# Kernel optimization log

Measured on AMD Instinct MI355X. Metric: run time of the kernel, lower is better.

Reference implementation:

```python
import jax, jax.numpy as jnp
import numpy as np

NEG_SLOPE = 0.01  # F.leaky_relu default


def gcn_conv(x, W, b, src, dst):
    """PyG GCNConv: add self-loops, symmetric deg^-1/2 normalization, linear, scatter-add."""
    n = x.shape[0]
    loop = jnp.arange(n)
    s = jnp.concatenate([src, loop])  # source j
    d = jnp.concatenate([dst, loop])  # target i
    deg = jax.ops.segment_sum(jnp.ones_like(d, dtype=x.dtype), d, num_segments=n)
    dis = jnp.where(deg > 0, jax.lax.rsqrt(jnp.maximum(deg, 1e-12)), 0.0)
    norm = dis[s] * dis[d]                       # [E+N]
    h = x @ W                                    # [N, out]
    msg = h[s] * norm[:, None]                   # gather + scale
    out = jax.ops.segment_sum(msg, d, num_segments=n)  # scatter-add to targets
    return out + b


def setup_inputs() -> dict:
    key = jax.random.key(0)
    ks = jax.random.split(key, 8)
    N, E, G = 100000, 800000, 100
    IN, H, OUT = 128, 256, 16
    x = jax.random.normal(ks[0], (N, IN), dtype=jnp.float32)
    edge_index = jax.random.randint(ks[1], (2, E), 0, N, dtype=jnp.int64)
    batch = jnp.repeat(jnp.arange(G, dtype=jnp.int64), N // G)  # sorted graph ids
    def glorot(k, fi, fo):
        lim = np.sqrt(6.0 / (fi + fo))
        return jax.random.uniform(k, (fi, fo), jnp.float32, -lim, lim)
    return {
        "x": x, "edge_index": edge_index, "batch": batch,
        "W1": glorot(ks[2], IN, H), "b1": jnp.zeros((H,), jnp.float32),
        "W2": glorot(ks[3], H, H),  "b2": jnp.zeros((H,), jnp.float32),
        "W3": glorot(ks[4], H, OUT), "b3": jnp.zeros((OUT,), jnp.float32),
    }


def reference(x, edge_index, batch, W1, b1, W2, b2, W3, b3):
    src, dst = edge_index[0], edge_index[1]
    h = gcn_conv(x, W1, b1, src, dst)
    h = jax.nn.leaky_relu(h, NEG_SLOPE)  # dropout p=0.0 -> identity
    h = gcn_conv(h, W2, b2, src, dst)
    h = jax.nn.leaky_relu(h, NEG_SLOPE)
    h = gcn_conv(h, W3, b3, src, dst)
    # get_zero_nodes: first node of each graph in the sorted batch vector
    mask = jnp.concatenate([jnp.array([True]), batch[1:] != batch[:-1]])
    return h[mask, :]  # [n_graphs, out_channels]
```

## Files before the change

kernel.cpp:

```cpp
#include <hip/hip_runtime.h>

#define NEG_SLOPE 0.01f

using short8 = __attribute__((ext_vector_type(8))) short;
using f32x4  = __attribute__((ext_vector_type(4))) float;

__device__ inline float b2f(ushort u) {
    union { unsigned u; float f; } x; x.u = ((unsigned)u) << 16; return x.f;
}
__device__ inline ushort f2b(float f) {
    union { float f; unsigned u; } x; x.f = f;
    unsigned r = x.u + 0x7FFFu + ((x.u >> 16) & 1u);
    return (ushort)(r >> 16);
}
__device__ inline void gload16(const void* g, void* l) {
    __builtin_amdgcn_global_load_lds((__attribute__((address_space(1))) void*)g,
                                     (__attribute__((address_space(3))) void*)l, 16, 0, 0);
}


__global__ void init_kernel(const int* __restrict__ batch, int* __restrict__ cnt,
                            int* __restrict__ flag1, int* __restrict__ flag2,
                            int* __restrict__ rootflag, int* __restrict__ picked, int N) {
    int i = blockIdx.x * blockDim.x + threadIdx.x;
    if (i >= N) return;
    cnt[i] = 0;
    int root = (i == 0) || (batch[i] != batch[i - 1]);
    flag1[i] = root;
    flag2[i] = 0;
    rootflag[i] = root;
    if (root) picked[batch[i]] = i;
}


__global__ void count_f1(const int* __restrict__ src, const int* __restrict__ dst,
                         const int* __restrict__ rootflag, int* __restrict__ cnt,
                         int* __restrict__ flag1, int E) {
    int i = blockIdx.x * blockDim.x + threadIdx.x;
    int e0 = i * 4;
    if (e0 + 3 < E) {
        int4 dq = *(const int4*)(dst + e0);
        int r0 = rootflag[dq.x], r1 = rootflag[dq.y], r2 = rootflag[dq.z], r3 = rootflag[dq.w];
        atomicAdd(&cnt[dq.x], 1);
        atomicAdd(&cnt[dq.y], 1);
        atomicAdd(&cnt[dq.z], 1);
        atomicAdd(&cnt[dq.w], 1);
        if (r0 | r1 | r2 | r3) {
            int4 sq = *(const int4*)(src + e0);
            if (r0) flag1[sq.x] = 1;
            if (r1) flag1[sq.y] = 1;
            if (r2) flag1[sq.z] = 1;
            if (r3) flag1[sq.w] = 1;
        }
    } else if (e0 < E) {
        for (int e = e0; e < E; e++) {
            int d = dst[e];
            atomicAdd(&cnt[d], 1);
            if (rootflag[d]) flag1[src[e]] = 1;
        }
    }
}


__global__ void frontier2v(const int* __restrict__ src, const int* __restrict__ dst,
                           const int* __restrict__ flag1, int* __restrict__ flag2,
                           int E, int N) {
    int i = blockIdx.x * blockDim.x + threadIdx.x;
    int e0 = i * 4;
    if (e0 + 3 < E) {
        int4 dq = *(const int4*)(dst + e0);
        int f0 = flag1[dq.x], f1 = flag1[dq.y], f2 = flag1[dq.z], f3 = flag1[dq.w];
        if (f0 | f1 | f2 | f3) {
            int4 sq = *(const int4*)(src + e0);
            if (f0) flag2[sq.x] = 1;
            if (f1) flag2[sq.y] = 1;
            if (f2) flag2[sq.z] = 1;
            if (f3) flag2[sq.w] = 1;
        }
    } else if (e0 < E) {
        for (int e = e0; e < E; e++) if (flag1[dst[e]]) flag2[src[e]] = 1;
    }
    if (i < N && flag1[i]) flag2[i] = 1;
}


__global__ __launch_bounds__(256) void tscan1w(const int* __restrict__ cnt,
                                               const int* __restrict__ f1,
                                               const int* __restrict__ f2,
                                               int4* __restrict__ bsums,
                                               float* __restrict__ dis, int N, int nb,
                                               const float* __restrict__ W1, ushort* __restrict__ W1t,
                                               const float* __restrict__ W2, ushort* __restrict__ W2t) {
    __shared__ int l0[256], l1[256], l2[256];
    int b = blockIdx.x, t = threadIdx.x;
    if (b < nb) {
        int base = b * 1024 + t * 4;
        int c[4] = {0,0,0,0}, a1[4] = {0,0,0,0}, a2[4] = {0,0,0,0};
        if (base + 3 < N) {
            int4 q = *(const int4*)(cnt + base); c[0]=q.x; c[1]=q.y; c[2]=q.z; c[3]=q.w;
            int4 u = *(const int4*)(f1 + base);  a1[0]=u.x; a1[1]=u.y; a1[2]=u.z; a1[3]=u.w;
            int4 v = *(const int4*)(f2 + base);  a2[0]=v.x; a2[1]=v.y; a2[2]=v.z; a2[3]=v.w;
        } else {
            for (int i = 0; i < 4; i++) if (base + i < N) {
                c[i] = cnt[base + i]; a1[i] = f1[base + i]; a2[i] = f2[base + i];
            }
        }
#pragma unroll
        for (int i = 0; i < 4; i++)
            if (base + i < N) dis[base + i] = rsqrtf((float)c[i] + 1.0f);
        int s0 = 0, s1 = 0, s2 = 0;
#pragma unroll
        for (int i = 0; i < 4; i++) { s0 += a2[i] ? c[i] : 0; s1 += a1[i]; s2 += a2[i]; }
        l0[t] = s0; l1[t] = s1; l2[t] = s2;
        __syncthreads();
        for (int off = 128; off > 0; off >>= 1) {
            if (t < off) { l0[t] += l0[t + off]; l1[t] += l1[t + off]; l2[t] += l2[t + off]; }
            __syncthreads();
        }
        if (t == 0) bsums[b] = make_int4(l0[0], l1[0], l2[0], 0);
    }
    for (int idx = b * 256 + t; idx < 98304; idx += gridDim.x * 256) {
        if (idx < 32768) {
            int n = idx >> 7, k = idx & 127;
            W1t[idx] = f2b(W1[k * 256 + n]);
        } else {
            int j = idx - 32768;
            int n = j >> 8, k = j & 255;
            W2t[j] = f2b(W2[k * 256 + n]);
        }
    }
}

__global__ __launch_bounds__(1024) void tscan2(int4* __restrict__ bsums, int* __restrict__ counts,
                                               int* __restrict__ rowptr, int N, int nb) {
    __shared__ int l0[1024], l1[1024], l2[1024];
    int t = threadIdx.x;
    int v0 = 0, v1 = 0, v2 = 0;
    if (t < nb) { int4 v = bsums[t]; v0 = v.x; v1 = v.y; v2 = v.z; }
    l0[t] = v0; l1[t] = v1; l2[t] = v2;
    __syncthreads();
    for (int off = 1; off < 1024; off <<= 1) {
        int u0 = (t >= off) ? l0[t - off] : 0;
        int u1 = (t >= off) ? l1[t - off] : 0;
        int u2 = (t >= off) ? l2[t - off] : 0;
        __syncthreads();
        l0[t] += u0; l1[t] += u1; l2[t] += u2;
        __syncthreads();
    }
    if (t < nb) bsums[t] = make_int4(l0[t] - v0, l1[t] - v1, l2[t] - v2, 0);
    if (t == 1023) {
        counts[0] = l1[1023];
        counts[1] = l2[1023];
        rowptr[N] = l0[1023];
    }
}

__global__ __launch_bounds__(256) void tscan3(const int* __restrict__ cnt,
                                              const int* __restrict__ f1,
                                              const int* __restrict__ f2,
                                              const int4* __restrict__ bsums,
                                              int* __restrict__ rowptr, int* __restrict__ cur,
                                              int* __restrict__ pos1, int* __restrict__ pos2,
                                              int* __restrict__ list1, int* __restrict__ list2,
                                              int N) {
    __shared__ int l0[256], l1[256], l2[256];
    int b = blockIdx.x, t = threadIdx.x;
    int base = b * 1024 + t * 4;
    int c[4] = {0,0,0,0}, a1[4] = {0,0,0,0}, a2[4] = {0,0,0,0};
    if (base + 3 < N) {
        int4 q = *(const int4*)(cnt + base); c[0]=q.x; c[1]=q.y; c[2]=q.z; c[3]=q.w;
        int4 u = *(const int4*)(f1 + base);  a1[0]=u.x; a1[1]=u.y; a1[2]=u.z; a1[3]=u.w;
        int4 v = *(const int4*)(f2 + base);  a2[0]=v.x; a2[1]=v.y; a2[2]=v.z; a2[3]=v.w;
    } else {
        for (int i = 0; i < 4; i++) if (base + i < N) {
            c[i] = cnt[base + i]; a1[i] = f1[base + i]; a2[i] = f2[base + i];
        }
    }
    int m[4];
#pragma unroll
    for (int i = 0; i < 4; i++) m[i] = a2[i] ? c[i] : 0;
    int s0 = m[0] + m[1] + m[2] + m[3];
    int s1 = a1[0] + a1[1] + a1[2] + a1[3];
    int s2 = a2[0] + a2[1] + a2[2] + a2[3];
    l0[t] = s0; l1[t] = s1; l2[t] = s2;
    __syncthreads();
    for (int off = 1; off < 256; off <<= 1) {
        int u0 = (t >= off) ? l0[t - off] : 0;
        int u1 = (t >= off) ? l1[t - off] : 0;
        int u2 = (t >= off) ? l2[t - off] : 0;
        __syncthreads();
        l0[t] += u0; l1[t] += u1; l2[t] += u2;
        __syncthreads();
    }
    int4 bs = bsums[b];
    int run0 = bs.x + l0[t] - s0;
    int run1 = bs.y + l1[t] - s1;
    int run2 = bs.z + l2[t] - s2;
#pragma unroll
    for (int i = 0; i < 4; i++) {
        if (base + i < N) {
            rowptr[base + i] = run0;
            cur[base + i] = run0;
            if (a1[i]) { pos1[base + i] = run1; list1[run1] = base + i; }
            if (a2[i]) { pos2[base + i] = run2; list2[run2] = base + i; }
        }
        run0 += m[i]; run1 += a1[i]; run2 += a2[i];
    }
}


__global__ void fill_fv(const int* __restrict__ src, const int* __restrict__ dst,
                        const int* __restrict__ flag2, int* __restrict__ cur,
                        int* __restrict__ col, int E) {
    int i = blockIdx.x * blockDim.x + threadIdx.x;
    int e0 = i * 4;
    if (e0 + 3 < E) {
        int4 dq = *(const int4*)(dst + e0);
        int f0 = flag2[dq.x], f1 = flag2[dq.y], f2 = flag2[dq.z], f3 = flag2[dq.w];
        if (f0 | f1 | f2 | f3) {
            int4 sq = *(const int4*)(src + e0);
            if (f0) col[atomicAdd(&cur[dq.x], 1)] = sq.x;
            if (f1) col[atomicAdd(&cur[dq.y], 1)] = sq.y;
            if (f2) col[atomicAdd(&cur[dq.z], 1)] = sq.z;
            if (f3) col[atomicAdd(&cur[dq.w], 1)] = sq.w;
        }
    } else if (e0 < E) {
        for (int e = e0; e < E; e++) {
            int d = dst[e];
            if (flag2[d]) col[atomicAdd(&cur[d], 1)] = src[e];
        }
    }
}


__global__ __launch_bounds__(256) void aggx_c(const float* __restrict__ x,
                                              const float* __restrict__ dis,
                                              const int* __restrict__ rowptr,
                                              const int* __restrict__ col,
                                              const int* __restrict__ list2,
                                              const int* __restrict__ counts,
                                              ushort* __restrict__ aggXc) {
    const int M2 = counts[1];
    int wave = blockIdx.x * 4 + (threadIdx.x >> 6);
    int lane = threadIdx.x & 63;
    int li = lane & 31, sub = lane >> 5;
    int stride = gridDim.x * 8;
    const float* xp = x + li * 4;
    for (int p = wave * 2 + sub; p < M2; p += stride) {
        int node = list2[p];
        float di = dis[node];
        float4 sv = *(const float4*)(xp + (size_t)node * 128);
        float a0 = di * sv.x, a1 = di * sv.y, a2 = di * sv.z, a3 = di * sv.w;
        int e = rowptr[node], e1 = rowptr[node + 1];
        for (; e + 2 <= e1; e += 2) {
            int s0 = col[e], s1 = col[e + 1];
            float w0 = dis[s0], w1 = dis[s1];
            float4 v0 = *(const float4*)(xp + (size_t)s0 * 128);
            float4 v1 = *(const float4*)(xp + (size_t)s1 * 128);
            a0 += w0 * v0.x + w1 * v1.x;
            a1 += w0 * v0.y + w1 * v1.y;
            a2 += w0 * v0.z + w1 * v1.z;
            a3 += w0 * v0.w + w1 * v1.w;
        }
        if (e < e1) {
            int s = col[e];
            float w = dis[s];
            float4 v = *(const float4*)(xp + (size_t)s * 128);
            a0 += w * v.x; a1 += w * v.y; a2 += w * v.z; a3 += w * v.w;
        }
        ushort4 o;
        o.x = f2b(di * a0); o.y = f2b(di * a1); o.z = f2b(di * a2); o.w = f2b(di * a3);
        *(ushort4*)(aggXc + (size_t)p * 128 + li * 4) = o;
    }
}


__global__ __launch_bounds__(256) void agg2_c(const ushort* __restrict__ h1c,
                                              const float* __restrict__ dis,
                                              const int* __restrict__ rowptr,
                                              const int* __restrict__ col,
                                              const int* __restrict__ list1,
                                              const int* __restrict__ pos2,
                                              const int* __restrict__ counts,
                                              ushort* __restrict__ agg1c) {
    const int M1 = counts[0];
    int wave = blockIdx.x * 4 + (threadIdx.x >> 6);
    int lane = threadIdx.x & 63;
    int li = lane & 31, sub = lane >> 5;
    int stride = gridDim.x * 8;
    const ushort* hp = h1c + (size_t)li * 8;
    for (int p = wave * 2 + sub; p < M1; p += stride) {
        int i = list1[p];
        float di = dis[i];
        float a[8];
        {
            short8 v = *(const short8*)(hp + (size_t)pos2[i] * 256);
#pragma unroll
            for (int j = 0; j < 8; j++) a[j] = b2f((ushort)v[j]);
        }
        int e1 = rowptr[i + 1];
        for (int e = rowptr[i]; e < e1; e++) {
            short8 v = *(const short8*)(hp + (size_t)pos2[col[e]] * 256);
#pragma unroll
            for (int j = 0; j < 8; j++) a[j] += b2f((ushort)v[j]);
        }
        short8 o;
#pragma unroll
        for (int j = 0; j < 8; j++) o[j] = (short)f2b(di * a[j]);
        *(short8*)(agg1c + (size_t)p * 256 + li * 8) = o;
    }
}


template <int K>
__global__ __launch_bounds__(512) void gemm_c(const ushort* __restrict__ A,
                                              const ushort* __restrict__ Bt,
                                              const float* __restrict__ bias,
                                              const float* __restrict__ dis,
                                              const int* __restrict__ list,
                                              const int* __restrict__ counts, int which,
                                              ushort* __restrict__ C) {
    __shared__ ushort As[128 * 64];
    __shared__ ushort Bs[256 * 64];
    const int M = counts[which];
    const int t = threadIdx.x;
    const int lane = t & 63;
    const int w = t >> 6;
    const int wm = w >> 2, wn = w & 3;

    for (int tile = blockIdx.x; tile * 128 < M; tile += gridDim.x) {
        const int row0 = tile * 128;
        f32x4 acc[4][4] = {};

        for (int kt = 0; kt < K / 64; kt++) {
#pragma unroll
            for (int it = 0; it < 2; it++) {
                int q = it * 512 + t;
                int r = q >> 3, c = q & 7;
                int cs = c ^ (r & 7);
                int ga = min(row0 + r, M - 1);
                gload16(A + (size_t)ga * K + kt * 64 + cs * 8, &As[q * 8]);
            }
#pragma unroll
            for (int it = 0; it < 4; it++) {
                int q = it * 512 + t;
                int r = q >> 3, c = q & 7;
                int cs = c ^ (r & 7);
                gload16(Bt + (size_t)r * K + kt * 64 + cs * 8, &Bs[q * 8]);
            }
            __syncthreads();
#pragma unroll
            for (int ks = 0; ks < 2; ks++) {
                short8 a[4], b[4];
                int cc = ks * 4 + (lane >> 4);
#pragma unroll
                for (int m = 0; m < 4; m++) {
                    int R = wm * 64 + m * 16 + (lane & 15);
                    a[m] = *(const short8*)&As[R * 64 + ((cc ^ (R & 7)) * 8)];
                }
#pragma unroll
                for (int n = 0; n < 4; n++) {
                    int R = wn * 64 + n * 16 + (lane & 15);
                    b[n] = *(const short8*)&Bs[R * 64 + ((cc ^ (R & 7)) * 8)];
                }
#pragma unroll
                for (int m = 0; m < 4; m++)
#pragma unroll
                    for (int n = 0; n < 4; n++)
                        acc[m][n] = __builtin_amdgcn_mfma_f32_16x16x32_bf16(a[m], b[n], acc[m][n], 0, 0, 0);
            }
            __syncthreads();
        }

#pragma unroll
        for (int m = 0; m < 4; m++) {
#pragma unroll
            for (int j = 0; j < 4; j++) {
                int grow = row0 + wm * 64 + m * 16 + (lane >> 4) * 4 + j;
                if (grow >= M) continue;
                float dr = dis[list[grow]];
#pragma unroll
                for (int n = 0; n < 4; n++) {
                    int gcol = wn * 64 + n * 16 + (lane & 15);
                    float v = acc[m][n][j] + bias[gcol];
                    v = v > 0.f ? v : NEG_SLOPE * v;
                    C[(size_t)grow * 256 + gcol] = f2b(v * dr);
                }
            }
        }
    }
}


__global__ __launch_bounds__(256) void final_c(const ushort* __restrict__ h2c,
                                               const float* __restrict__ dis,
                                               const int* __restrict__ rowptr,
                                               const int* __restrict__ col,
                                               const int* __restrict__ picked,
                                               const int* __restrict__ pos1,
                                               const float* __restrict__ W3,
                                               const float* __restrict__ b3,
                                               float* __restrict__ out, int G) {
    __shared__ float agg[256];
    __shared__ float red[256];
    int g = blockIdx.x;
    int t = threadIdx.x;
    if (g >= G) return;
    int i = picked[g];
    float di = dis[i];
    float a = b2f(h2c[(size_t)pos1[i] * 256 + t]);
    int e1 = rowptr[i + 1];
    for (int e = rowptr[i]; e < e1; e++) {
        a += b2f(h2c[(size_t)pos1[col[e]] * 256 + t]);
    }
    agg[t] = di * a;
    __syncthreads();
    int c = t & 15, seg = t >> 4;
    float p = 0.f;
#pragma unroll
    for (int kk = 0; kk < 16; kk++) {
        int k = seg * 16 + kk;
        p += agg[k] * W3[k * 16 + c];
    }
    red[t] = p;
    __syncthreads();
    if (t < 16) {
        float sres = 0.f;
#pragma unroll
        for (int ss = 0; ss < 16; ss++) sres += red[ss * 16 + t];
        out[g * 16 + t] = sres + b3[t];
    }
}


extern "C" void kernel_launch(void* const* d_in, const int* in_sizes, int n_in,
                              void* d_out, int out_size, void* d_ws, size_t ws_size,
                              hipStream_t stream) {
    const float* x   = (const float*)d_in[0];
    const int* ei    = (const int*)d_in[1];
    const int* batch = (const int*)d_in[2];
    const float* W1  = (const float*)d_in[3];
    const float* b1  = (const float*)d_in[4];
    const float* W2  = (const float*)d_in[5];
    const float* b2  = (const float*)d_in[6];
    const float* W3  = (const float*)d_in[7];
    const float* b3  = (const float*)d_in[8];

    const int IN = 128, H = 256, OUT = 16;
    int N = in_sizes[0] / IN;
    int E = in_sizes[1] / 2;
    int G = out_size / OUT;
    const int* srcp = ei;
    const int* dstp = ei + E;

    char* p = (char*)d_ws;
    auto carve = [&](size_t bytes) {
        char* q = p;
        p += (bytes + 255) & ~(size_t)255;
        return q;
    };
    int*    cnt      = (int*)carve((size_t)N * 4);
    int*    flag1    = (int*)carve((size_t)N * 4);
    int*    flag2    = (int*)carve((size_t)N * 4);
    int*    rootflag = (int*)carve((size_t)N * 4);
    float*  dis    = (float*)carve((size_t)N * 4);
    int*    rowptr = (int*)carve(((size_t)N + 1) * 4);
    int*    cur    = (int*)carve((size_t)N * 4);
    int4*   tbsums = (int4*)carve(1024 * 16);
    int*    counts = (int*)carve(256);
    int*    picked = (int*)carve((size_t)G * 4);
    int*    pos1   = (int*)carve((size_t)N * 4);
    int*    pos2   = (int*)carve((size_t)N * 4);
    int*    list1  = (int*)carve((size_t)N * 4);
    int*    list2  = (int*)carve((size_t)N * 4);
    int*    col    = (int*)carve((size_t)E * 4);
    ushort* W1t    = (ushort*)carve((size_t)256 * 128 * 2);
    ushort* W2t    = (ushort*)carve((size_t)256 * 256 * 2);
    ushort* RA     = (ushort*)carve((size_t)N * H * 2);
    ushort* RB     = (ushort*)carve((size_t)N * H * 2);

    ushort* aggXc = RA;
    ushort* agg1c = RA;
    ushort* h1c   = RB;
    ushort* h2c   = RB;

    int nb = (N + 1023) / 1024;
    int e4 = (E + 3) / 4;
    int epN = (e4 > N ? e4 : N);
    int scanw_grid = (nb > 384 ? nb : 384);

    init_kernel<<<(N + 255) / 256, 256, 0, stream>>>(batch, cnt, flag1, flag2, rootflag, picked, N);

    count_f1<<<(e4 + 255) / 256, 256, 0, stream>>>(srcp, dstp, rootflag, cnt, flag1, E);

    frontier2v<<<(epN + 255) / 256, 256, 0, stream>>>(srcp, dstp, flag1, flag2, E, N);

    tscan1w<<<scanw_grid, 256, 0, stream>>>(cnt, flag1, flag2, tbsums, dis, N, nb, W1, W1t, W2, W2t);
    tscan2<<<1, 1024, 0, stream>>>(tbsums, counts, rowptr, N, nb);
    tscan3<<<nb, 256, 0, stream>>>(cnt, flag1, flag2, tbsums, rowptr, cur, pos1, pos2, list1, list2, N);

    fill_fv<<<(e4 + 255) / 256, 256, 0, stream>>>(srcp, dstp, flag2, cur, col, E);

    aggx_c<<<1024, 256, 0, stream>>>(x, dis, rowptr, col, list2, counts, aggXc);
    gemm_c<128><<<256, 512, 0, stream>>>(aggXc, W1t, b1, dis, list2, counts, 1, h1c);

    agg2_c<<<128, 256, 0, stream>>>(h1c, dis, rowptr, col, list1, pos2, counts, agg1c);
    gemm_c<256><<<64, 512, 0, stream>>>(agg1c, W2t, b2, dis, list1, counts, 0, h2c);

    final_c<<<G, 256, 0, stream>>>(h2c, dis, rowptr, col, picked, pos1, W3, b3, (float*)d_out, G);
}
```

Baseline: 134.1 us.

## Fuse three-pass scan into single-pass decoupled lookback scan

```diff
diff --git a/kernel.cpp b/kernel.cpp
--- a/kernel.cpp
+++ b/kernel.cpp
@@ -21,8 +21,10 @@
 
 __global__ void init_kernel(const int* __restrict__ batch, int* __restrict__ cnt,
                             int* __restrict__ flag1, int* __restrict__ flag2,
-                            int* __restrict__ rootflag, int* __restrict__ picked, int N) {
+                            int* __restrict__ rootflag, int* __restrict__ picked,
+                            int4* __restrict__ aggslot, int N) {
     int i = blockIdx.x * blockDim.x + threadIdx.x;
+    if (i < 1024) aggslot[i] = make_int4(0, 0, 0, 0);
     if (i >= N) return;
     cnt[i] = 0;
     int root = (i == 0) || (batch[i] != batch[i - 1]);
@@ -84,41 +86,101 @@
 }
 
 
-__global__ __launch_bounds__(256) void tscan1w(const int* __restrict__ cnt,
-                                               const int* __restrict__ f1,
-                                               const int* __restrict__ f2,
-                                               int4* __restrict__ bsums,
-                                               float* __restrict__ dis, int N, int nb,
-                                               const float* __restrict__ W1, ushort* __restrict__ W1t,
-                                               const float* __restrict__ W2, ushort* __restrict__ W2t) {
+__global__ __launch_bounds__(256) void scan_one(
+    const int* __restrict__ cnt, const int* __restrict__ f1, const int* __restrict__ f2,
+    int4* __restrict__ aggslot, float* __restrict__ dis,
+    int* __restrict__ rowptr, int* __restrict__ cur,
+    int* __restrict__ pos1, int* __restrict__ pos2,
+    int* __restrict__ list1, int* __restrict__ list2,
+    int* __restrict__ counts, int N, int nb,
+    const float* __restrict__ W1, ushort* __restrict__ W1t,
+    const float* __restrict__ W2, ushort* __restrict__ W2t) {
     __shared__ int l0[256], l1[256], l2[256];
-    int b = blockIdx.x, t = threadIdx.x;
-    if (b < nb) {
-        int base = b * 1024 + t * 4;
-        int c[4] = {0,0,0,0}, a1[4] = {0,0,0,0}, a2[4] = {0,0,0,0};
-        if (base + 3 < N) {
-            int4 q = *(const int4*)(cnt + base); c[0]=q.x; c[1]=q.y; c[2]=q.z; c[3]=q.w;
-            int4 u = *(const int4*)(f1 + base);  a1[0]=u.x; a1[1]=u.y; a1[2]=u.z; a1[3]=u.w;
-            int4 v = *(const int4*)(f2 + base);  a2[0]=v.x; a2[1]=v.y; a2[2]=v.z; a2[3]=v.w;
-        } else {
-            for (int i = 0; i < 4; i++) if (base + i < N) {
-                c[i] = cnt[base + i]; a1[i] = f1[base + i]; a2[i] = f2[base + i];
+    __shared__ int baseS[3];
+    const int b = blockIdx.x, t = threadIdx.x;
+    const int base = b * 1024 + t * 4;
+
+    int c[4] = {0,0,0,0}, a1[4] = {0,0,0,0}, a2[4] = {0,0,0,0};
+    if (base + 3 < N) {
+        int4 q = *(const int4*)(cnt + base); c[0]=q.x; c[1]=q.y; c[2]=q.z; c[3]=q.w;
+        int4 u = *(const int4*)(f1 + base);  a1[0]=u.x; a1[1]=u.y; a1[2]=u.z; a1[3]=u.w;
+        int4 v = *(const int4*)(f2 + base);  a2[0]=v.x; a2[1]=v.y; a2[2]=v.z; a2[3]=v.w;
+    } else {
+        for (int i = 0; i < 4; i++) if (base + i < N) {
+            c[i] = cnt[base + i]; a1[i] = f1[base + i]; a2[i] = f2[base + i];
+        }
+    }
+#pragma unroll
+    for (int i = 0; i < 4; i++)
+        if (base + i < N) dis[base + i] = rsqrtf((float)c[i] + 1.0f);
+
+    int m[4];
+#pragma unroll
+    for (int i = 0; i < 4; i++) m[i] = a2[i] ? c[i] : 0;
+    int ts0 = m[0] + m[1] + m[2] + m[3];
+    int ts1 = a1[0] + a1[1] + a1[2] + a1[3];
+    int ts2 = a2[0] + a2[1] + a2[2] + a2[3];
+    l0[t] = ts0; l1[t] = ts1; l2[t] = ts2;
+    __syncthreads();
+    for (int off = 1; off < 256; off <<= 1) {
+        int u0 = (t >= off) ? l0[t - off] : 0;
+        int u1 = (t >= off) ? l1[t - off] : 0;
+        int u2 = (t >= off) ? l2[t - off] : 0;
+        __syncthreads();
+        l0[t] += u0; l1[t] += u1; l2[t] += u2;
+        __syncthreads();
+    }
+
+    if (t == 0) {
+        __hip_atomic_store(&aggslot[b].x, l0[255], __ATOMIC_RELAXED, __HIP_MEMORY_SCOPE_AGENT);
+        __hip_atomic_store(&aggslot[b].y, l1[255], __ATOMIC_RELAXED, __HIP_MEMORY_SCOPE_AGENT);
+        __hip_atomic_store(&aggslot[b].z, l2[255], __ATOMIC_RELAXED, __HIP_MEMORY_SCOPE_AGENT);
+        __hip_atomic_store(&aggslot[b].w, 1, __ATOMIC_RELEASE, __HIP_MEMORY_SCOPE_AGENT);
+    }
+
+    if (t < 64) {
+        int g0 = 0, g1 = 0, g2 = 0;
+        for (int w0 = 0; w0 < b; w0 += 64) {
+            int idx = w0 + t;
+            if (idx < b) {
+                while (__hip_atomic_load(&aggslot[idx].w, __ATOMIC_ACQUIRE,
+                                         __HIP_MEMORY_SCOPE_AGENT) == 0) {
+                    __builtin_amdgcn_s_sleep(1);
+                }
+                g0 += __hip_atomic_load(&aggslot[idx].x, __ATOMIC_RELAXED, __HIP_MEMORY_SCOPE_AGENT);
+                g1 += __hip_atomic_load(&aggslot[idx].y, __ATOMIC_RELAXED, __HIP_MEMORY_SCOPE_AGENT);
+                g2 += __hip_atomic_load(&aggslot[idx].z, __ATOMIC_RELAXED, __HIP_MEMORY_SCOPE_AGENT);
             }
         }
 #pragma unroll
-        for (int i = 0; i < 4; i++)
-            if (base + i < N) dis[base + i] = rsqrtf((float)c[i] + 1.0f);
-        int s0 = 0, s1 = 0, s2 = 0;
-#pragma unroll
-        for (int i = 0; i < 4; i++) { s0 += a2[i] ? c[i] : 0; s1 += a1[i]; s2 += a2[i]; }
-        l0[t] = s0; l1[t] = s1; l2[t] = s2;
-        __syncthreads();
-        for (int off = 128; off > 0; off >>= 1) {
-            if (t < off) { l0[t] += l0[t + off]; l1[t] += l1[t + off]; l2[t] += l2[t + off]; }
-            __syncthreads();
-        }
-        if (t == 0) bsums[b] = make_int4(l0[0], l1[0], l2[0], 0);
-    }
+        for (int s = 1; s < 64; s <<= 1) {
+            g0 += __shfl_xor(g0, s, 64);
+            g1 += __shfl_xor(g1, s, 64);
+            g2 += __shfl_xor(g2, s, 64);
+        }
+        if (t == 0) { baseS[0] = g0; baseS[1] = g1; baseS[2] = g2; }
+    }
+    __syncthreads();
+
+    int run0 = baseS[0] + l0[t] - ts0;
+    int run1 = baseS[1] + l1[t] - ts1;
+    int run2 = baseS[2] + l2[t] - ts2;
+#pragma unroll
+    for (int i = 0; i < 4; i++) {
+        if (base + i < N) {
+            rowptr[base + i] = run0;
+            cur[base + i] = run0;
+            if (a1[i]) { pos1[base + i] = run1; list1[run1] = base + i; }
+            if (a2[i]) { pos2[base + i] = run2; list2[run2] = base + i; }
+        }
+        run0 += m[i]; run1 += a1[i]; run2 += a2[i];
+    }
+    if (b == nb - 1 && t == 255) {
+        counts[0] = baseS[1] + l1[255];
+        counts[1] = baseS[2] + l2[255];
+        rowptr[N] = baseS[0] + l0[255];
+    }
+
     for (int idx = b * 256 + t; idx < 98304; idx += gridDim.x * 256) {
         if (idx < 32768) {
             int n = idx >> 7, k = idx & 127;
@@ -128,83 +190,6 @@
             int n = j >> 8, k = j & 255;
             W2t[j] = f2b(W2[k * 256 + n]);
         }
-    }
-}
-
-__global__ __launch_bounds__(1024) void tscan2(int4* __restrict__ bsums, int* __restrict__ counts,
-                                               int* __restrict__ rowptr, int N, int nb) {
-    __shared__ int l0[1024], l1[1024], l2[1024];
-    int t = threadIdx.x;
-    int v0 = 0, v1 = 0, v2 = 0;
-    if (t < nb) { int4 v = bsums[t]; v0 = v.x; v1 = v.y; v2 = v.z; }
-    l0[t] = v0; l1[t] = v1; l2[t] = v2;
-    __syncthreads();
-    for (int off = 1; off < 1024; off <<= 1) {
-        int u0 = (t >= off) ? l0[t - off] : 0;
-        int u1 = (t >= off) ? l1[t - off] : 0;
-        int u2 = (t >= off) ? l2[t - off] : 0;
-        __syncthreads();
-        l0[t] += u0; l1[t] += u1; l2[t] += u2;
-        __syncthreads();
-    }
-    if (t < nb) bsums[t] = make_int4(l0[t] - v0, l1[t] - v1, l2[t] - v2, 0);
-    if (t == 1023) {
-        counts[0] = l1[1023];
-        counts[1] = l2[1023];
-        rowptr[N] = l0[1023];
-    }
-}
-
-__global__ __launch_bounds__(256) void tscan3(const int* __restrict__ cnt,
-                                              const int* __restrict__ f1,
-                                              const int* __restrict__ f2,
-                                              const int4* __restrict__ bsums,
-                                              int* __restrict__ rowptr, int* __restrict__ cur,
-                                              int* __restrict__ pos1, int* __restrict__ pos2,
-                                              int* __restrict__ list1, int* __restrict__ list2,
-                                              int N) {
-    __shared__ int l0[256], l1[256], l2[256];
-    int b = blockIdx.x, t = threadIdx.x;
-    int base = b * 1024 + t * 4;
-    int c[4] = {0,0,0,0}, a1[4] = {0,0,0,0}, a2[4] = {0,0,0,0};
-    if (base + 3 < N) {
-        int4 q = *(const int4*)(cnt + base); c[0]=q.x; c[1]=q.y; c[2]=q.z; c[3]=q.w;
-        int4 u = *(const int4*)(f1 + base);  a1[0]=u.x; a1[1]=u.y; a1[2]=u.z; a1[3]=u.w;
-        int4 v = *(const int4*)(f2 + base);  a2[0]=v.x; a2[1]=v.y; a2[2]=v.z; a2[3]=v.w;
-    } else {
-        for (int i = 0; i < 4; i++) if (base + i < N) {
-            c[i] = cnt[base + i]; a1[i] = f1[base + i]; a2[i] = f2[base + i];
-        }
-    }
-    int m[4];
-#pragma unroll
-    for (int i = 0; i < 4; i++) m[i] = a2[i] ? c[i] : 0;
-    int s0 = m[0] + m[1] + m[2] + m[3];
-    int s1 = a1[0] + a1[1] + a1[2] + a1[3];
-    int s2 = a2[0] + a2[1] + a2[2] + a2[3];
-    l0[t] = s0; l1[t] = s1; l2[t] = s2;
-    __syncthreads();
-    for (int off = 1; off < 256; off <<= 1) {
-        int u0 = (t >= off) ? l0[t - off] : 0;
-        int u1 = (t >= off) ? l1[t - off] : 0;
-        int u2 = (t >= off) ? l2[t - off] : 0;
-        __syncthreads();
-        l0[t] += u0; l1[t] += u1; l2[t] += u2;
-        __syncthreads();
-    }
-    int4 bs = bsums[b];
-    int run0 = bs.x + l0[t] - s0;
-    int run1 = bs.y + l1[t] - s1;
-    int run2 = bs.z + l2[t] - s2;
-#pragma unroll
-    for (int i = 0; i < 4; i++) {
-        if (base + i < N) {
-            rowptr[base + i] = run0;
-            cur[base + i] = run0;
-            if (a1[i]) { pos1[base + i] = run1; list1[run1] = base + i; }
-            if (a2[i]) { pos2[base + i] = run2; list2[run2] = base + i; }
-        }
-        run0 += m[i]; run1 += a1[i]; run2 += a2[i];
     }
 }
 
@@ -466,7 +451,7 @@
     float*  dis    = (float*)carve((size_t)N * 4);
     int*    rowptr = (int*)carve(((size_t)N + 1) * 4);
     int*    cur    = (int*)carve((size_t)N * 4);
-    int4*   tbsums = (int4*)carve(1024 * 16);
+    int4*   aggslot= (int4*)carve(1024 * 16);
     int*    counts = (int*)carve(256);
     int*    picked = (int*)carve((size_t)G * 4);
     int*    pos1   = (int*)carve((size_t)N * 4);
@@ -487,25 +472,18 @@
     int nb = (N + 1023) / 1024;
     int e4 = (E + 3) / 4;
     int epN = (e4 > N ? e4 : N);
-    int scanw_grid = (nb > 384 ? nb : 384);
-
-    init_kernel<<<(N + 255) / 256, 256, 0, stream>>>(batch, cnt, flag1, flag2, rootflag, picked, N);
-
+
+    init_kernel<<<(N + 255) / 256, 256, 0, stream>>>(batch, cnt, flag1, flag2, rootflag,
+                                                     picked, aggslot, N);
     count_f1<<<(e4 + 255) / 256, 256, 0, stream>>>(srcp, dstp, rootflag, cnt, flag1, E);
-
     frontier2v<<<(epN + 255) / 256, 256, 0, stream>>>(srcp, dstp, flag1, flag2, E, N);
-
-    tscan1w<<<scanw_grid, 256, 0, stream>>>(cnt, flag1, flag2, tbsums, dis, N, nb, W1, W1t, W2, W2t);
-    tscan2<<<1, 1024, 0, stream>>>(tbsums, counts, rowptr, N, nb);
-    tscan3<<<nb, 256, 0, stream>>>(cnt, flag1, flag2, tbsums, rowptr, cur, pos1, pos2, list1, list2, N);
-
+    scan_one<<<nb, 256, 0, stream>>>(cnt, flag1, flag2, aggslot, dis, rowptr, cur,
+                                     pos1, pos2, list1, list2, counts, N, nb,
+                                     W1, W1t, W2, W2t);
     fill_fv<<<(e4 + 255) / 256, 256, 0, stream>>>(srcp, dstp, flag2, cur, col, E);
-
     aggx_c<<<1024, 256, 0, stream>>>(x, dis, rowptr, col, list2, counts, aggXc);
-    gemm_c<128><<<256, 512, 0, stream>>>(aggXc, W1t, b1, dis, list2, counts, 1, h1c);
-
+    gemm_c<128><<<128, 512, 0, stream>>>(aggXc, W1t, b1, dis, list2, counts, 1, h1c);
     agg2_c<<<128, 256, 0, stream>>>(h1c, dis, rowptr, col, list1, pos2, counts, agg1c);
     gemm_c<256><<<64, 512, 0, stream>>>(agg1c, W2t, b2, dis, list1, counts, 0, h2c);
-
     final_c<<<G, 256, 0, stream>>>(h2c, dis, rowptr, col, picked, pos1, W3, b3, (float*)d_out, G);
 }
```

Measured after the change: 131.3 us, median of 2. 1.02x faster.
